# Optimization experiments

Hardware: AMD Instinct MI355X
Metric: run time of the kernel (lower is better)

The kernel has to match this reference:

```python
import jax, jax.numpy as jnp
import numpy as np

VAR_EPS = 1e-5
CLAMP = 1e-7
B, S, D = 128, 1024, 256  # D = ambient Lorentz dim (time + D-1 spatial), k = 1


def linner(a, b):
    """Minkowski inner product <a,b>_L = -a0*b0 + sum_i a_i*b_i, keepdims."""
    return -a[..., :1] * b[..., :1] + jnp.sum(a[..., 1:] * b[..., 1:], axis=-1, keepdims=True)


def add_origin(x):
    # x + o where o = (1, 0, ..., 0)
    return jnp.concatenate([x[..., :1] + 1.0, x[..., 1:]], axis=-1)


def centroid(x):
    """Lorentz centroid over dim -2 (k=1): normalize the Euclidean mean back to the hyperboloid."""
    avg = jnp.mean(x, axis=-2)
    denom = jnp.sqrt(jnp.clip(jnp.abs(-linner(avg, avg)), 1e-8, None))
    return avg / denom


def logmap(x, y):
    alpha = jnp.clip(-linner(x, y), 1.0 + CLAMP, None)
    u = y - alpha * x
    return (jnp.arccosh(alpha) / jnp.sqrt(alpha * alpha - 1.0)) * u


def transp0back(x, v):
    # parallel transport from x to origin o: v - v0/(1+x0) * (x+o)
    coef = v[..., :1] / (1.0 + x[..., :1])
    return v - coef * add_origin(x)


def transp0(y, v):
    # parallel transport from origin o to y: v + <y,v>_L/(1+y0) * (o+y)
    coef = linner(y, v) / (1.0 + y[..., :1])
    return v + coef * add_origin(y)


def expmap(x, u):
    n = jnp.sqrt(jnp.clip(linner(u, u), CLAMP, None))
    return jnp.cosh(n) * x + jnp.sinh(n) * (u / n)


def expmap0_space(u_space):
    # exp map at origin from a purely-spatial tangent vector (used only for data generation)
    n = jnp.sqrt(jnp.clip(jnp.sum(u_space * u_space, axis=-1, keepdims=True), CLAMP, None))
    return jnp.concatenate([jnp.cosh(n), jnp.sinh(n) * (u_space / n)], axis=-1)


def setup_inputs() -> dict:
    key = jax.random.key(0)
    k1, = jax.random.split(key, 1)
    u_space = 0.5 * jax.random.normal(k1, (B, S, D - 1), dtype=jnp.float32)
    x = expmap0_space(u_space)  # valid points on the hyperboloid, [B,S,D]
    beta = jnp.zeros((D,), dtype=jnp.float32).at[0].set(1.0)  # manifold.origin
    gamma = jnp.ones((1,), dtype=jnp.float32)
    return {"x": x, "beta": beta, "gamma": gamma}


def reference(x, beta, gamma):
    # training-mode forward of LorentzBatchNorm_beta (3D input path)
    mean = centroid(centroid(x))            # [D] Frechet-style centroid over seq then batch
    x_t = logmap(mean, x)                   # [B,S,D] tangent at mean
    x_t = transp0back(mean, x_t)            # transport to tangent at origin
    var = jnp.sqrt(jnp.var(x_t, axis=(0, 1)) + VAR_EPS)  # [D] per-feature std
    x_t = x_t * (gamma / var)
    x_t = transp0(beta, x_t)                # transport to tangent at beta
    return expmap(beta, x_t)                # [B,S,D] back on the manifold
```

## Files before the change

kernel.cpp:

```cpp
#include <hip/hip_runtime.h>
#include <math.h>

#define BB 128
#define SS 1024
#define DD 256
#define NP (BB * SS)
#define CH 16
#define ROWS (SS / CH)
#define NB3 2048
#define NW3 (NB3 * 4)
#define RB4 32
#define NB4A (NB3 / RB4)

#define LN2F 0.69314718056f
#define L2EF 1.44269504089f
__device__ __forceinline__ float fsqrt(float x) { return __builtin_amdgcn_sqrtf(x); }
__device__ __forceinline__ float frcp(float x)  { return __builtin_amdgcn_rcpf(x); }
__device__ __forceinline__ float frsq(float x)  { return __builtin_amdgcn_rsqf(x); }
__device__ __forceinline__ float flog2(float x) { return __builtin_amdgcn_logf(x); }
__device__ __forceinline__ float fexp2(float x) { return __builtin_amdgcn_exp2f(x); }

__device__ __forceinline__ float wave_sum(float v) {
#pragma unroll
    for (int m = 32; m >= 1; m >>= 1) v += __shfl_xor(v, m, 64);
    return v;
}

__device__ __forceinline__ float block_sum(float v, float* red) {
    const int t = threadIdx.x;
    red[t] = v;
    __syncthreads();
#pragma unroll
    for (int off = 128; off >= 1; off >>= 1) {
        if (t < off) red[t] += red[t + off];
        __syncthreads();
    }
    float r = red[0];
    __syncthreads();
    return r;
}

__global__ __launch_bounds__(256) void k1_partial(const float* __restrict__ x,
                                                  float* __restrict__ part) {
    const int ch = blockIdx.x, b = blockIdx.y;
    const int w = threadIdx.x >> 6, l = threadIdx.x & 63;
    const float4* x4 = (const float4*)x;
    size_t base = ((size_t)b * SS + (size_t)ch * ROWS + (size_t)w * (ROWS / 4)) * (DD / 4);
    float4 s = make_float4(0.f, 0.f, 0.f, 0.f);
#pragma unroll 4
    for (int r = 0; r < ROWS / 4; ++r) {
        float4 v = x4[base + (size_t)r * (DD / 4) + l];
        s.x += v.x; s.y += v.y; s.z += v.z; s.w += v.w;
    }
    __shared__ float lds[4][DD];
    lds[w][4 * l + 0] = s.x; lds[w][4 * l + 1] = s.y;
    lds[w][4 * l + 2] = s.z; lds[w][4 * l + 3] = s.w;
    __syncthreads();
    const int t = threadIdx.x;
    part[((size_t)b * CH + ch) * DD + t] = lds[0][t] + lds[1][t] + lds[2][t] + lds[3][t];
}

__global__ __launch_bounds__(256) void k2a_c1(const float* __restrict__ part,
                                              float* __restrict__ c1) {
    const int b = blockIdx.x;
    const int t = threadIdx.x;
    __shared__ float red[DD];
    float sx = 0.f;
#pragma unroll
    for (int ch = 0; ch < CH; ++ch) sx += part[((size_t)b * CH + ch) * DD + t];
    float avg = sx * (1.0f / SS);
    float contrib = (t == 0) ? avg * avg : -avg * avg;
    float r = block_sum(contrib, red);
    c1[(size_t)b * DD + t] = avg * frsq(fmaxf(fabsf(r), 1e-8f));
}

__global__ __launch_bounds__(256) void k2b_mean(const float* __restrict__ c1,
                                                float* __restrict__ wsmean) {
    const int t = threadIdx.x;
    __shared__ float red[DD];
    float acc = 0.f;
#pragma unroll 8
    for (int b = 0; b < BB; ++b) acc += c1[(size_t)b * DD + t];
    float avg = acc * (1.0f / BB);
    float contrib = (t == 0) ? avg * avg : -avg * avg;
    float r = block_sum(contrib, red);
    wsmean[t] = avg * frsq(fmaxf(fabsf(r), 1e-8f));
}

__device__ __forceinline__ float4 compute_xt(const float4* __restrict__ row, int l,
                                             float4 m4, float m0, float inv1pm0) {
    float4 v = row[l];
    float dp = fmaf(v.x, m4.x, fmaf(v.y, m4.y, fmaf(v.z, m4.z, v.w * m4.w)));
    float dot = wave_sum(dp);
    float y0 = __shfl(v.x, 0, 64);
    float alpha = fmaxf(fmaf(2.0f * m0, y0, -dot), 1.0f + 1e-7f);
    float t = fmaf(alpha, alpha, -1.0f);
    float f = (LN2F * flog2(alpha + fsqrt(t))) * frsq(t);
    float xt0 = f * (y0 - alpha * m0);
    float coef = xt0 * inv1pm0;
    float4 r;
    r.x = f * (v.x - alpha * m4.x) - coef * ((l == 0) ? (m0 + 1.0f) : m4.x);
    r.y = f * (v.y - alpha * m4.y) - coef * m4.y;
    r.z = f * (v.z - alpha * m4.z) - coef * m4.z;
    r.w = f * (v.w - alpha * m4.w) - coef * m4.w;
    return r;
}

__global__ __launch_bounds__(256) void k3_stats(const float* __restrict__ x,
                                                const float* __restrict__ wsmean,
                                                float* __restrict__ part3) {
    const int w = threadIdx.x >> 6, l = threadIdx.x & 63;
    float4 m4 = ((const float4*)wsmean)[l];
    float m0 = wsmean[0];
    float inv1pm0 = frcp(1.0f + m0);
    float4 s = make_float4(0, 0, 0, 0), q = make_float4(0, 0, 0, 0);
    const int wid = blockIdx.x * 4 + w;
#pragma unroll 2
    for (int p = wid; p < NP; p += NW3) {
        const float4* row = ((const float4*)x) + (size_t)p * (DD / 4);
        float4 t4 = compute_xt(row, l, m4, m0, inv1pm0);
        s.x += t4.x; s.y += t4.y; s.z += t4.z; s.w += t4.w;
        q.x += t4.x * t4.x; q.y += t4.y * t4.y; q.z += t4.z * t4.z; q.w += t4.w * t4.w;
    }
    __shared__ float lds[4][2 * DD];
    lds[w][4 * l + 0] = s.x; lds[w][4 * l + 1] = s.y;
    lds[w][4 * l + 2] = s.z; lds[w][4 * l + 3] = s.w;
    lds[w][DD + 4 * l + 0] = q.x; lds[w][DD + 4 * l + 1] = q.y;
    lds[w][DD + 4 * l + 2] = q.z; lds[w][DD + 4 * l + 3] = q.w;
    __syncthreads();
    const int t = threadIdx.x;
    part3[(size_t)blockIdx.x * (2 * DD) + t]      = lds[0][t] + lds[1][t] + lds[2][t] + lds[3][t];
    part3[(size_t)blockIdx.x * (2 * DD) + DD + t] = lds[0][DD + t] + lds[1][DD + t] + lds[2][DD + t] + lds[3][DD + t];
}

__global__ __launch_bounds__(512) void k4a_reduce(const float* __restrict__ part3,
                                                  float* __restrict__ stage2) {
    const int t = threadIdx.x;
    const int r0 = blockIdx.x * RB4;
    float s = 0.f;
#pragma unroll 8
    for (int r = 0; r < RB4; ++r) s += part3[(size_t)(r0 + r) * (2 * DD) + t];
    stage2[(size_t)blockIdx.x * (2 * DD) + t] = s;
}

__global__ __launch_bounds__(256) void k4b_scale(const float* __restrict__ stage2,
                                                 const float* __restrict__ gamma,
                                                 float* __restrict__ wsscale) {
    const int t = threadIdx.x;
    double s1 = 0.0, s2 = 0.0;
    for (int i = 0; i < NB4A; ++i) {
        s1 += (double)stage2[(size_t)i * (2 * DD) + t];
        s2 += (double)stage2[(size_t)i * (2 * DD) + DD + t];
    }
    const double N = (double)NP;
    double mv = s1 / N;
    double var = s2 / N - mv * mv;
    wsscale[t] = gamma[0] * frsq((float)var + 1e-5f);
}

__global__ __launch_bounds__(256) void k5_out(const float* __restrict__ x,
                                              const float* __restrict__ wsmean,
                                              const float* __restrict__ wsscale,
                                              const float* __restrict__ beta,
                                              float4* __restrict__ out4) {
    const int w = threadIdx.x >> 6, l = threadIdx.x & 63;
    float4 m4 = ((const float4*)wsmean)[l];
    float m0 = wsmean[0];
    float inv1pm0 = frcp(1.0f + m0);
    float4 sc = ((const float4*)wsscale)[l];
    float4 b4 = ((const float4*)beta)[l];
    float b0 = beta[0];
    float inv1pb0 = frcp(1.0f + b0);
    const int wid = blockIdx.x * 4 + w;
#pragma unroll 2
    for (int p = wid; p < NP; p += NW3) {
        const float4* row = ((const float4*)x) + (size_t)p * (DD / 4);
        float4 t4 = compute_xt(row, l, m4, m0, inv1pm0);
        float4 v = make_float4(t4.x * sc.x, t4.y * sc.y, t4.z * sc.z, t4.w * sc.w);
        float dpb = fmaf(v.x, b4.x, fmaf(v.y, b4.y, fmaf(v.z, b4.z, v.w * b4.w)));
        float dotb = wave_sum(dpb);
        float v0 = __shfl(v.x, 0, 64);
        float coef = (dotb - 2.0f * b0 * v0) * inv1pb0;
        float4 wv;
        wv.x = v.x + coef * ((l == 0) ? (b0 + 1.0f) : b4.x);
        wv.y = v.y + coef * b4.y;
        wv.z = v.z + coef * b4.z;
        wv.w = v.w + coef * b4.w;
        float dq = fmaf(wv.x, wv.x, fmaf(wv.y, wv.y, fmaf(wv.z, wv.z, wv.w * wv.w)));
        float dotw = wave_sum(dq);
        float w0 = v0 + coef * (b0 + 1.0f);
        float nn = fmaxf(dotw - 2.0f * w0 * w0, 1e-7f);
        float n = fsqrt(nn);
        float e = fexp2(n * L2EF);
        float ei = frcp(e);
        float chn = 0.5f * (e + ei);
        float shn = 0.5f * (e - ei) * frsq(nn);
        float4 o;
        o.x = chn * ((l == 0) ? b0 : b4.x) + shn * wv.x;
        o.y = chn * b4.y + shn * wv.y;
        o.z = chn * b4.z + shn * wv.z;
        o.w = chn * b4.w + shn * wv.w;
        out4[(size_t)p * (DD / 4) + l] = o;
    }
}

extern "C" void kernel_launch(void* const* d_in, const int* in_sizes, int n_in,
                              void* d_out, int out_size, void* d_ws, size_t ws_size,
                              hipStream_t stream) {
    (void)in_sizes; (void)n_in; (void)out_size; (void)ws_size;
    const float* x     = (const float*)d_in[0];
    const float* beta  = (const float*)d_in[1];
    const float* gamma = (const float*)d_in[2];
    float* out = (float*)d_out;

    float* wsmean  = (float*)d_ws;
    float* wsscale = wsmean + DD;

    float* part   = out;
    float* c1     = out + (size_t)BB * CH * DD;
    float* part3  = out;
    float* stage2 = out + (size_t)NB3 * 2 * DD;

    k1_partial<<<dim3(CH, BB), 256, 0, stream>>>(x, part);
    k2a_c1<<<BB, 256, 0, stream>>>(part, c1);
    k2b_mean<<<1, 256, 0, stream>>>(c1, wsmean);
    k3_stats<<<NB3, 256, 0, stream>>>(x, wsmean, part3);
    k4a_reduce<<<NB4A, 512, 0, stream>>>(part3, stage2);
    k4b_scale<<<1, 256, 0, stream>>>(stage2, gamma, wsscale);
    k5_out<<<NB3, 256, 0, stream>>>(x, wsmean, wsscale, beta, (float4*)out);
}
```

Before: 106.1 us.

## Process two rows per wave with half-wave reductions and nontemporal output stores

Each 64-lane wave now handles two rows at once, each lane owning two float4s, so the cross-lane reductions shrink from 6 to 5 shuffle steps and each wave does half as many reduction rounds. The output kernel writes with nontemporal stores, and the stats and output kernels get a minimum-occupancy launch bound. Scratch buffers move from the output buffer into the workspace, so the output is no longer reused as temporary storage. The trade-off is higher register pressure per lane and reliance on the workspace being large enough to hold the scratch data.

```diff
diff --git a/kernel.cpp b/kernel.cpp
--- a/kernel.cpp
+++ b/kernel.cpp
@@ -12,6 +12,8 @@
 #define RB4 32
 #define NB4A (NB3 / RB4)
 
+typedef float fx4 __attribute__((ext_vector_type(4)));
+
 #define LN2F 0.69314718056f
 #define L2EF 1.44269504089f
 __device__ __forceinline__ float fsqrt(float x) { return __builtin_amdgcn_sqrtf(x); }
@@ -20,9 +22,9 @@
 __device__ __forceinline__ float flog2(float x) { return __builtin_amdgcn_logf(x); }
 __device__ __forceinline__ float fexp2(float x) { return __builtin_amdgcn_exp2f(x); }
 
-__device__ __forceinline__ float wave_sum(float v) {
-#pragma unroll
-    for (int m = 32; m >= 1; m >>= 1) v += __shfl_xor(v, m, 64);
+__device__ __forceinline__ float half_sum(float v) {
+#pragma unroll
+    for (int m = 16; m >= 1; m >>= 1) v += __shfl_xor(v, m, 64);
     return v;
 }
 
@@ -38,6 +40,10 @@
     float r = red[0];
     __syncthreads();
     return r;
+}
+
+__device__ __forceinline__ float dot4(float4 a, float4 b) {
+    return fmaf(a.x, b.x, fmaf(a.y, b.y, fmaf(a.z, b.z, a.w * b.w)));
 }
 
 __global__ __launch_bounds__(256) void k1_partial(const float* __restrict__ x,
@@ -87,50 +93,62 @@
     wsmean[t] = avg * frsq(fmaxf(fabsf(r), 1e-8f));
 }
 
-__device__ __forceinline__ float4 compute_xt(const float4* __restrict__ row, int l,
-                                             float4 m4, float m0, float inv1pm0) {
-    float4 v = row[l];
-    float dp = fmaf(v.x, m4.x, fmaf(v.y, m4.y, fmaf(v.z, m4.z, v.w * m4.w)));
-    float dot = wave_sum(dp);
-    float y0 = __shfl(v.x, 0, 64);
+__device__ __forceinline__ void compute_xt_h(float4 va, float4 vb, int j, int srcl,
+                                             float4 ma, float4 mb, float m0, float inv1pm0,
+                                             float4& ra, float4& rb) {
+    float dp = dot4(va, ma) + dot4(vb, mb);
+    float dot = half_sum(dp);
+    float y0 = __shfl(va.x, srcl, 64);
     float alpha = fmaxf(fmaf(2.0f * m0, y0, -dot), 1.0f + 1e-7f);
-    float t = fmaf(alpha, alpha, -1.0f);
-    float f = (LN2F * flog2(alpha + fsqrt(t))) * frsq(t);
+    float tt = fmaf(alpha, alpha, -1.0f);
+    float f = (LN2F * flog2(alpha + fsqrt(tt))) * frsq(tt);
     float xt0 = f * (y0 - alpha * m0);
     float coef = xt0 * inv1pm0;
-    float4 r;
-    r.x = f * (v.x - alpha * m4.x) - coef * ((l == 0) ? (m0 + 1.0f) : m4.x);
-    r.y = f * (v.y - alpha * m4.y) - coef * m4.y;
-    r.z = f * (v.z - alpha * m4.z) - coef * m4.z;
-    r.w = f * (v.w - alpha * m4.w) - coef * m4.w;
-    return r;
-}
-
-__global__ __launch_bounds__(256) void k3_stats(const float* __restrict__ x,
-                                                const float* __restrict__ wsmean,
-                                                float* __restrict__ part3) {
+    ra.x = f * (va.x - alpha * ma.x) - coef * ((j == 0) ? (m0 + 1.0f) : ma.x);
+    ra.y = f * (va.y - alpha * ma.y) - coef * ma.y;
+    ra.z = f * (va.z - alpha * ma.z) - coef * ma.z;
+    ra.w = f * (va.w - alpha * ma.w) - coef * ma.w;
+    rb.x = f * (vb.x - alpha * mb.x) - coef * mb.x;
+    rb.y = f * (vb.y - alpha * mb.y) - coef * mb.y;
+    rb.z = f * (vb.z - alpha * mb.z) - coef * mb.z;
+    rb.w = f * (vb.w - alpha * mb.w) - coef * mb.w;
+}
+
+__global__ __launch_bounds__(256, 8) void k3_stats(const float* __restrict__ x,
+                                                   const float* __restrict__ wsmean,
+                                                   float* __restrict__ part3) {
     const int w = threadIdx.x >> 6, l = threadIdx.x & 63;
-    float4 m4 = ((const float4*)wsmean)[l];
+    const int j = l & 31, h = l >> 5, srcl = l & 32;
+    float4 ma = ((const float4*)wsmean)[2 * j];
+    float4 mb = ((const float4*)wsmean)[2 * j + 1];
     float m0 = wsmean[0];
     float inv1pm0 = frcp(1.0f + m0);
-    float4 s = make_float4(0, 0, 0, 0), q = make_float4(0, 0, 0, 0);
+    float4 sa = make_float4(0, 0, 0, 0), sb = sa, qa = sa, qb = sa;
     const int wid = blockIdx.x * 4 + w;
 #pragma unroll 2
-    for (int p = wid; p < NP; p += NW3) {
+    for (int p = 2 * wid + h; p < NP; p += 2 * NW3) {
         const float4* row = ((const float4*)x) + (size_t)p * (DD / 4);
-        float4 t4 = compute_xt(row, l, m4, m0, inv1pm0);
-        s.x += t4.x; s.y += t4.y; s.z += t4.z; s.w += t4.w;
-        q.x += t4.x * t4.x; q.y += t4.y * t4.y; q.z += t4.z * t4.z; q.w += t4.w * t4.w;
-    }
-    __shared__ float lds[4][2 * DD];
-    lds[w][4 * l + 0] = s.x; lds[w][4 * l + 1] = s.y;
-    lds[w][4 * l + 2] = s.z; lds[w][4 * l + 3] = s.w;
-    lds[w][DD + 4 * l + 0] = q.x; lds[w][DD + 4 * l + 1] = q.y;
-    lds[w][DD + 4 * l + 2] = q.z; lds[w][DD + 4 * l + 3] = q.w;
-    __syncthreads();
-    const int t = threadIdx.x;
-    part3[(size_t)blockIdx.x * (2 * DD) + t]      = lds[0][t] + lds[1][t] + lds[2][t] + lds[3][t];
-    part3[(size_t)blockIdx.x * (2 * DD) + DD + t] = lds[0][DD + t] + lds[1][DD + t] + lds[2][DD + t] + lds[3][DD + t];
+        float4 va = row[2 * j], vb = row[2 * j + 1];
+        float4 ta, tb;
+        compute_xt_h(va, vb, j, srcl, ma, mb, m0, inv1pm0, ta, tb);
+        sa.x += ta.x; sa.y += ta.y; sa.z += ta.z; sa.w += ta.w;
+        sb.x += tb.x; sb.y += tb.y; sb.z += tb.z; sb.w += tb.w;
+        qa.x += ta.x * ta.x; qa.y += ta.y * ta.y; qa.z += ta.z * ta.z; qa.w += ta.w * ta.w;
+        qb.x += tb.x * tb.x; qb.y += tb.y * tb.y; qb.z += tb.z * tb.z; qb.w += tb.w * tb.w;
+    }
+    __shared__ float lds[8][2 * DD];
+    const int r = w * 2 + h;
+    ((float4*)&lds[r][8 * j])[0] = sa;
+    ((float4*)&lds[r][8 * j])[1] = sb;
+    ((float4*)&lds[r][DD + 8 * j])[0] = qa;
+    ((float4*)&lds[r][DD + 8 * j])[1] = qb;
+    __syncthreads();
+    const int t = threadIdx.x;
+    float accs = 0.f, accq = 0.f;
+#pragma unroll
+    for (int rr = 0; rr < 8; ++rr) { accs += lds[rr][t]; accq += lds[rr][DD + t]; }
+    part3[(size_t)blockIdx.x * (2 * DD) + t] = accs;
+    part3[(size_t)blockIdx.x * (2 * DD) + DD + t] = accq;
 }
 
 __global__ __launch_bounds__(512) void k4a_reduce(const float* __restrict__ part3,
@@ -158,49 +176,67 @@
     wsscale[t] = gamma[0] * frsq((float)var + 1e-5f);
 }
 
-__global__ __launch_bounds__(256) void k5_out(const float* __restrict__ x,
-                                              const float* __restrict__ wsmean,
-                                              const float* __restrict__ wsscale,
-                                              const float* __restrict__ beta,
-                                              float4* __restrict__ out4) {
+__global__ __launch_bounds__(256, 8) void k5_out(const float* __restrict__ x,
+                                                 const float* __restrict__ wsmean,
+                                                 const float* __restrict__ wsscale,
+                                                 const float* __restrict__ beta,
+                                                 float* __restrict__ out) {
     const int w = threadIdx.x >> 6, l = threadIdx.x & 63;
-    float4 m4 = ((const float4*)wsmean)[l];
+    const int j = l & 31, h = l >> 5, srcl = l & 32;
+    float4 ma = ((const float4*)wsmean)[2 * j];
+    float4 mb = ((const float4*)wsmean)[2 * j + 1];
     float m0 = wsmean[0];
     float inv1pm0 = frcp(1.0f + m0);
-    float4 sc = ((const float4*)wsscale)[l];
-    float4 b4 = ((const float4*)beta)[l];
+    float4 sca = ((const float4*)wsscale)[2 * j];
+    float4 scb = ((const float4*)wsscale)[2 * j + 1];
+    float4 ba = ((const float4*)beta)[2 * j];
+    float4 bb = ((const float4*)beta)[2 * j + 1];
     float b0 = beta[0];
     float inv1pb0 = frcp(1.0f + b0);
+    float b0p1 = b0 + 1.0f;
     const int wid = blockIdx.x * 4 + w;
 #pragma unroll 2
-    for (int p = wid; p < NP; p += NW3) {
+    for (int p = 2 * wid + h; p < NP; p += 2 * NW3) {
         const float4* row = ((const float4*)x) + (size_t)p * (DD / 4);
-        float4 t4 = compute_xt(row, l, m4, m0, inv1pm0);
-        float4 v = make_float4(t4.x * sc.x, t4.y * sc.y, t4.z * sc.z, t4.w * sc.w);
-        float dpb = fmaf(v.x, b4.x, fmaf(v.y, b4.y, fmaf(v.z, b4.z, v.w * b4.w)));
-        float dotb = wave_sum(dpb);
-        float v0 = __shfl(v.x, 0, 64);
-        float coef = (dotb - 2.0f * b0 * v0) * inv1pb0;
-        float4 wv;
-        wv.x = v.x + coef * ((l == 0) ? (b0 + 1.0f) : b4.x);
-        wv.y = v.y + coef * b4.y;
-        wv.z = v.z + coef * b4.z;
-        wv.w = v.w + coef * b4.w;
-        float dq = fmaf(wv.x, wv.x, fmaf(wv.y, wv.y, fmaf(wv.z, wv.z, wv.w * wv.w)));
-        float dotw = wave_sum(dq);
-        float w0 = v0 + coef * (b0 + 1.0f);
-        float nn = fmaxf(dotw - 2.0f * w0 * w0, 1e-7f);
+        float4 va = row[2 * j], vb = row[2 * j + 1];
+        float4 ta, tb;
+        compute_xt_h(va, vb, j, srcl, ma, mb, m0, inv1pm0, ta, tb);
+        ta.x *= sca.x; ta.y *= sca.y; ta.z *= sca.z; ta.w *= sca.w;
+        tb.x *= scb.x; tb.y *= scb.y; tb.z *= scb.z; tb.w *= scb.w;
+        float dpb = dot4(ta, ba) + dot4(tb, bb);
+        float dotb = half_sum(dpb);
+        float v0 = __shfl(ta.x, srcl, 64);
+        float coef = fmaf(-2.0f * b0, v0, dotb) * inv1pb0;
+        float4 wva, wvb;
+        wva.x = ta.x + coef * ((j == 0) ? b0p1 : ba.x);
+        wva.y = ta.y + coef * ba.y;
+        wva.z = ta.z + coef * ba.z;
+        wva.w = ta.w + coef * ba.w;
+        wvb.x = tb.x + coef * bb.x;
+        wvb.y = tb.y + coef * bb.y;
+        wvb.z = tb.z + coef * bb.z;
+        wvb.w = tb.w + coef * bb.w;
+        float dq = dot4(wva, wva) + dot4(wvb, wvb);
+        float dotw = half_sum(dq);
+        float w0 = fmaf(coef, b0p1, v0);
+        float nn = fmaxf(fmaf(-2.0f * w0, w0, dotw), 1e-7f);
         float n = fsqrt(nn);
         float e = fexp2(n * L2EF);
         float ei = frcp(e);
         float chn = 0.5f * (e + ei);
         float shn = 0.5f * (e - ei) * frsq(nn);
-        float4 o;
-        o.x = chn * ((l == 0) ? b0 : b4.x) + shn * wv.x;
-        o.y = chn * b4.y + shn * wv.y;
-        o.z = chn * b4.z + shn * wv.z;
-        o.w = chn * b4.w + shn * wv.w;
-        out4[(size_t)p * (DD / 4) + l] = o;
+        fx4 oa, ob;
+        oa.x = fmaf(chn, (j == 0) ? b0 : ba.x, shn * wva.x);
+        oa.y = fmaf(chn, ba.y, shn * wva.y);
+        oa.z = fmaf(chn, ba.z, shn * wva.z);
+        oa.w = fmaf(chn, ba.w, shn * wva.w);
+        ob.x = fmaf(chn, bb.x, shn * wvb.x);
+        ob.y = fmaf(chn, bb.y, shn * wvb.y);
+        ob.z = fmaf(chn, bb.z, shn * wvb.z);
+        ob.w = fmaf(chn, bb.w, shn * wvb.w);
+        fx4* o4 = (fx4*)(out + (size_t)p * DD);
+        __builtin_nontemporal_store(oa, &o4[2 * j]);
+        __builtin_nontemporal_store(ob, &o4[2 * j + 1]);
     }
 }
 
@@ -215,11 +251,12 @@
 
     float* wsmean  = (float*)d_ws;
     float* wsscale = wsmean + DD;
-
-    float* part   = out;
-    float* c1     = out + (size_t)BB * CH * DD;
-    float* part3  = out;
-    float* stage2 = out + (size_t)NB3 * 2 * DD;
+    float* scratch = wsscale + DD;
+
+    float* part   = scratch;
+    float* c1     = scratch + (size_t)BB * CH * DD;
+    float* part3  = scratch;
+    float* stage2 = scratch + (size_t)NB3 * 2 * DD;
 
     k1_partial<<<dim3(CH, BB), 256, 0, stream>>>(x, part);
     k2a_c1<<<BB, 256, 0, stream>>>(part, c1);
@@ -227,5 +264,5 @@
     k3_stats<<<NB3, 256, 0, stream>>>(x, wsmean, part3);
     k4a_reduce<<<NB4A, 512, 0, stream>>>(part3, stage2);
     k4b_scale<<<1, 256, 0, stream>>>(stage2, gamma, wsscale);
-    k5_out<<<NB3, 256, 0, stream>>>(x, wsmean, wsscale, beta, (float4*)out);
-}
+    k5_out<<<NB3, 256, 0, stream>>>(x, wsmean, wsscale, beta, out);
+}
```

Measured after the change: 152.2 us. 1.43x slower.
